# Optimization experiments

Hardware: AMD Instinct MI355X
Metric: run time of the kernel (lower is better)

The kernel has to match this reference:

```python
import jax, jax.numpy as jnp
import numpy as np

B, D, O, I = 64, 128, 512, 512


def setup_inputs() -> dict:
    key = jax.random.key(0)
    k1, k2, k3 = jax.random.split(key, 3)
    inp = jax.random.bernoulli(k1, 0.5, (B, D, I))            # binary activations
    weight_noise = jax.random.bernoulli(k2, 0.5, (D, O, I))   # sigmoid(W) > rand, binary
    # popcount of I fair coins has mean I/2, std sqrt(I)/2; center threshold there
    bias_noise = (I / 2.0 + (jnp.sqrt(I) / 2.0)
                  * jax.random.normal(k3, (D, O), dtype=jnp.float32))
    return {"input": inp, "weight_noise": weight_noise, "bias_noise": bias_noise}


def reference(input, weight_noise, bias_noise):
    # (weight_noise == input).sum(-1) over binary {0,1} tensors equals
    #   dot(w, x) + dot(1-w, 1-x) = I - sum(w) - sum(x) + 2 * dot(w, x)
    # which avoids materializing the (B, D, O, I) comparison tensor.
    x = input.astype(jnp.float32)          # (B, D, I)
    w = weight_noise.astype(jnp.float32)   # (D, O, I)
    dot = jnp.einsum('bdi,doi->bdo', x, w)               # per-direction binary GEMM
    act = (jnp.float32(I) - w.sum(-1)[None, :, :]        # (1, D, O)
           - x.sum(-1)[:, :, None]                        # (B, D, 1)
           + 2.0 * dot)                                   # match counts, (B, D, O)
    return act > bias_noise[None, :, :]                   # bool (B, D, O)
```

## Files before the change

### kernel.cpp

```cpp
#include <hip/hip_runtime.h>
#include <cstdint>

typedef unsigned long long u64;
typedef unsigned int u32;

#define BB 64
#define DD 128
#define OO 512
#define II 512
#define OT 64
#define XROWS (BB * DD)

__device__ __forceinline__ int detect_mode(const u32* __restrict__ w) {
    bool all01 = true, allf = true;
#pragma unroll
    for (int i = 0; i < 32; ++i) {
        u32 v = w[i];
        all01 = all01 && (v <= 1u);
        allf  = allf  && (v == 0u || v == 0x3F800000u);
    }
    return all01 ? 1 : (allf ? 2 : 0);
}

__device__ __forceinline__ u64 pack_row(const void* __restrict__ src,
                                        size_t elem0, int mode, int lane) {
    u64 my = 0;
    if (mode == 0) {
        u64 v = *(const u64*)((const uint8_t*)src + elem0 + (size_t)lane * 8);
#pragma unroll
        for (int j = 0; j < 8; ++j) {
            u64 bj = __ballot(((u32)(v >> (8 * j))) & 1u);
            if (lane == j) my = bj;
        }
    } else {
        const u32 sh = (mode == 1) ? 0u : 23u;
        const uint4* p = (const uint4*)((const u32*)src + elem0);
        uint4 v0 = p[lane];
        uint4 v1 = p[64 + lane];
        u32 b0 = (v0.x >> sh) & 1u, b1 = (v0.y >> sh) & 1u;
        u32 b2 = (v0.z >> sh) & 1u, b3 = (v0.w >> sh) & 1u;
        u32 b4 = (v1.x >> sh) & 1u, b5 = (v1.y >> sh) & 1u;
        u32 b6 = (v1.z >> sh) & 1u, b7 = (v1.w >> sh) & 1u;
        u64 w0 = __ballot(b0), w1 = __ballot(b1), w2 = __ballot(b2), w3 = __ballot(b3);
        u64 w4 = __ballot(b4), w5 = __ballot(b5), w6 = __ballot(b6), w7 = __ballot(b7);
        if (lane == 0) my = w0;  if (lane == 1) my = w1;
        if (lane == 2) my = w2;  if (lane == 3) my = w3;
        if (lane == 4) my = w4;  if (lane == 5) my = w5;
        if (lane == 6) my = w6;  if (lane == 7) my = w7;
    }
    return my;
}

__global__ __launch_bounds__(256)
void pack_x_kernel(const void* __restrict__ x, const void* __restrict__ w,
                   u64* __restrict__ packed) {
    const int gtid = blockIdx.x * 256 + threadIdx.x;
    const int row  = gtid >> 6;
    const int lane = threadIdx.x & 63;
    const int mode = detect_mode((const u32*)w);
    u64 my = pack_row(x, (size_t)row * II, mode, lane);
    if (lane < 8) packed[(size_t)row * 8 + lane] = my;
}

__global__ __launch_bounds__(256)
void fused_kernel(const void* __restrict__ w, const u64* __restrict__ px,
                  const float* __restrict__ bias, int* __restrict__ out) {
    __shared__ u64 wp[OT][9];
    __shared__ u64 xp[BB][8];

    const int tid  = threadIdx.x;
    const int blk  = blockIdx.x;
    const int d    = blk >> 3;
    const int o0   = (blk & 7) * OT;
    const int wv   = tid >> 6;
    const int lane = tid & 63;

    const int mode = detect_mode((const u32*)w);

#pragma unroll
    for (int r = 0; r < 16; ++r) {
        const int o = wv * 16 + r;
        u64 my = pack_row(w, ((size_t)(d * OO + o0 + o)) * II, mode, lane);
        if (lane < 8) wp[o][lane] = my;
    }
#pragma unroll
    for (int t = tid; t < BB * 8; t += 256) {
        int b = t >> 3, k = t & 7;
        xp[b][k] = px[(size_t)(b * DD + d) * 8 + k];
    }
    const float bv = bias[d * OO + o0 + (tid & 63)];
    __syncthreads();

    const int o  = tid & 63;
    const int b0 = (tid >> 6) * 16;

    u64 wr[8];
#pragma unroll
    for (int k = 0; k < 8; ++k) wr[k] = wp[o][k];

    int* outp = out + (size_t)d * OO + o0 + o;
#pragma unroll 4
    for (int bi = 0; bi < 16; ++bi) {
        const int b = b0 + bi;
        int m = 0;
#pragma unroll
        for (int k = 0; k < 8; ++k) m += __popcll(xp[b][k] ^ wr[k]);
        const float act = (float)(512 - m);
        outp[(size_t)b * (DD * OO)] = (act > bv) ? 1 : 0;
    }
}

extern "C" void kernel_launch(void* const* d_in, const int* in_sizes, int n_in,
                              void* d_out, int out_size, void* d_ws, size_t ws_size,
                              hipStream_t stream) {
    const void*  x    = d_in[0];
    const void*  w    = d_in[1];
    const float* bias = (const float*)d_in[2];
    int*         out  = (int*)d_out;
    u64*         px   = (u64*)d_ws;

    pack_x_kernel<<<XROWS / 4, 256, 0, stream>>>(x, w, px);
    fused_kernel<<<DD * (OO / OT), 256, 0, stream>>>(w, px, bias, out);
}
```

Baseline: 39.19 us.

## Fuse input packing into main kernel and remap blocks for XCD locality

Drops the separate pack_x kernel. Each block now packs its own 64 input rows for its direction d straight from global memory, which removes a launch and the round trip through the workspace. Each x row is now packed 8 times, once per o-tile block. To make that redundant read cheaper, block IDs are remapped so the 8 o-tiles of one d land on the same XCD and can share its L2. The added per-block packing work and the extra x reads are the cost.

```diff
diff --git a/kernel.cpp b/kernel.cpp
--- a/kernel.cpp
+++ b/kernel.cpp
@@ -9,7 +9,6 @@
 #define OO 512
 #define II 512
 #define OT 64
-#define XROWS (BB * DD)
 
 __device__ __forceinline__ int detect_mode(const u32* __restrict__ w) {
     bool all01 = true, allf = true;
@@ -52,26 +51,17 @@
 }
 
 __global__ __launch_bounds__(256)
-void pack_x_kernel(const void* __restrict__ x, const void* __restrict__ w,
-                   u64* __restrict__ packed) {
-    const int gtid = blockIdx.x * 256 + threadIdx.x;
-    const int row  = gtid >> 6;
-    const int lane = threadIdx.x & 63;
-    const int mode = detect_mode((const u32*)w);
-    u64 my = pack_row(x, (size_t)row * II, mode, lane);
-    if (lane < 8) packed[(size_t)row * 8 + lane] = my;
-}
-
-__global__ __launch_bounds__(256)
-void fused_kernel(const void* __restrict__ w, const u64* __restrict__ px,
-                  const float* __restrict__ bias, int* __restrict__ out) {
+void binlin_one(const void* __restrict__ x, const void* __restrict__ w,
+                const float* __restrict__ bias, int* __restrict__ out) {
     __shared__ u64 wp[OT][9];
     __shared__ u64 xp[BB][8];
 
     const int tid  = threadIdx.x;
-    const int blk  = blockIdx.x;
-    const int d    = blk >> 3;
-    const int o0   = (blk & 7) * OT;
+    const int bid  = blockIdx.x;
+    const int xcd = bid & 7;
+    const int idx = bid >> 3;
+    const int d   = xcd * 16 + (idx >> 3);
+    const int o0  = (idx & 7) * OT;
     const int wv   = tid >> 6;
     const int lane = tid & 63;
 
@@ -84,9 +74,10 @@
         if (lane < 8) wp[o][lane] = my;
     }
 #pragma unroll
-    for (int t = tid; t < BB * 8; t += 256) {
-        int b = t >> 3, k = t & 7;
-        xp[b][k] = px[(size_t)(b * DD + d) * 8 + k];
+    for (int r = 0; r < 16; ++r) {
+        const int b = wv * 16 + r;
+        u64 my = pack_row(x, ((size_t)(b * DD + d)) * II, mode, lane);
+        if (lane < 8) xp[b][lane] = my;
     }
     const float bv = bias[d * OO + o0 + (tid & 63)];
     __syncthreads();
@@ -117,8 +108,6 @@
     const void*  w    = d_in[1];
     const float* bias = (const float*)d_in[2];
     int*         out  = (int*)d_out;
-    u64*         px   = (u64*)d_ws;
 
-    pack_x_kernel<<<XROWS / 4, 256, 0, stream>>>(x, w, px);
-    fused_kernel<<<DD * (OO / OT), 256, 0, stream>>>(w, px, bias, out);
+    binlin_one<<<DD * (OO / OT), 256, 0, stream>>>(x, w, bias, out);
 }
```

Result: no change. 38.55 us (-1.6%).

## Stage weight tiles into LDS via direct global-to-LDS loads and remap blocks per XCD

Applied to the files above, without the earlier changes.

For byte-encoded inputs, the fused kernel now copies weight rows and packed activations straight into shared memory with global_load_lds in two 16KB halves, then packs bits from LDS using ballots. It also remaps block IDs so consecutive d values stay on the same XCD for L2 locality, and sets an occupancy hint on launch bounds. The goal is fewer per-lane global loads with better coalescing and cache reuse, at the cost of 16KB extra LDS per block, extra barriers, and serialized load/pack phases.

```diff
diff --git a/kernel.cpp b/kernel.cpp
--- a/kernel.cpp
+++ b/kernel.cpp
@@ -22,27 +22,31 @@
     return all01 ? 1 : (allf ? 2 : 0);
 }
 
+__device__ __forceinline__ u64 ballots8_bytes(u64 v, int lane) {
+    u64 keep = 0;
+#pragma unroll
+    for (int j = 0; j < 8; ++j) {
+        u64 bj = __ballot((u32)(v >> (8 * j)) & 1u);
+        if (lane == j) keep = bj;
+    }
+    return keep;
+}
+
 __device__ __forceinline__ u64 pack_row(const void* __restrict__ src,
                                         size_t elem0, int mode, int lane) {
     u64 my = 0;
     if (mode == 0) {
         u64 v = *(const u64*)((const uint8_t*)src + elem0 + (size_t)lane * 8);
-#pragma unroll
-        for (int j = 0; j < 8; ++j) {
-            u64 bj = __ballot(((u32)(v >> (8 * j))) & 1u);
-            if (lane == j) my = bj;
-        }
+        my = ballots8_bytes(v, lane);
     } else {
         const u32 sh = (mode == 1) ? 0u : 23u;
         const uint4* p = (const uint4*)((const u32*)src + elem0);
-        uint4 v0 = p[lane];
-        uint4 v1 = p[64 + lane];
-        u32 b0 = (v0.x >> sh) & 1u, b1 = (v0.y >> sh) & 1u;
-        u32 b2 = (v0.z >> sh) & 1u, b3 = (v0.w >> sh) & 1u;
-        u32 b4 = (v1.x >> sh) & 1u, b5 = (v1.y >> sh) & 1u;
-        u32 b6 = (v1.z >> sh) & 1u, b7 = (v1.w >> sh) & 1u;
-        u64 w0 = __ballot(b0), w1 = __ballot(b1), w2 = __ballot(b2), w3 = __ballot(b3);
-        u64 w4 = __ballot(b4), w5 = __ballot(b5), w6 = __ballot(b6), w7 = __ballot(b7);
+        uint4 a = p[lane];
+        uint4 b = p[64 + lane];
+        u64 w0 = __ballot((a.x >> sh) & 1u), w1 = __ballot((a.y >> sh) & 1u);
+        u64 w2 = __ballot((a.z >> sh) & 1u), w3 = __ballot((a.w >> sh) & 1u);
+        u64 w4 = __ballot((b.x >> sh) & 1u), w5 = __ballot((b.y >> sh) & 1u);
+        u64 w6 = __ballot((b.z >> sh) & 1u), w7 = __ballot((b.w >> sh) & 1u);
         if (lane == 0) my = w0;  if (lane == 1) my = w1;
         if (lane == 2) my = w2;  if (lane == 3) my = w3;
         if (lane == 4) my = w4;  if (lane == 5) my = w5;
@@ -51,45 +55,100 @@
     return my;
 }
 
+__device__ __forceinline__ void gload_lds16(const void* g, void* lds) {
+    __builtin_amdgcn_global_load_lds(
+        (const __attribute__((address_space(1))) void*)g,
+        (__attribute__((address_space(3))) void*)lds, 16, 0, 0);
+}
+
 __global__ __launch_bounds__(256)
 void pack_x_kernel(const void* __restrict__ x, const void* __restrict__ w,
-                   u64* __restrict__ packed) {
+                   u64* __restrict__ px) {
     const int gtid = blockIdx.x * 256 + threadIdx.x;
     const int row  = gtid >> 6;
     const int lane = threadIdx.x & 63;
     const int mode = detect_mode((const u32*)w);
     u64 my = pack_row(x, (size_t)row * II, mode, lane);
-    if (lane < 8) packed[(size_t)row * 8 + lane] = my;
+    if (lane < 8) px[(size_t)row * 8 + lane] = my;
 }
 
-__global__ __launch_bounds__(256)
-void fused_kernel(const void* __restrict__ w, const u64* __restrict__ px,
+__global__ __launch_bounds__(256, 4)
+void fused_kernel(const void* __restrict__ x, const void* __restrict__ w,
+                  const u64* __restrict__ px,
                   const float* __restrict__ bias, int* __restrict__ out) {
+    __shared__ u64 stage64[2048];
     __shared__ u64 wp[OT][9];
     __shared__ u64 xp[BB][8];
 
     const int tid  = threadIdx.x;
-    const int blk  = blockIdx.x;
-    const int d    = blk >> 3;
-    const int o0   = (blk & 7) * OT;
+    const int bid  = blockIdx.x;
+    const int xcd  = bid & 7;
+    const int idx  = bid >> 3;
+    const int d    = xcd * 16 + (idx >> 3);
+    const int o0   = (idx & 7) * OT;
     const int wv   = tid >> 6;
     const int lane = tid & 63;
 
     const int mode = detect_mode((const u32*)w);
+    const float bv = bias[d * OO + o0 + (tid & 63)];
+
+    uint8_t* stage = (uint8_t*)stage64;
+
+    if (mode == 0) {
+        const uint8_t* wtile = (const uint8_t*)w + (size_t)(d * OO + o0) * II;
 
 #pragma unroll
-    for (int r = 0; r < 16; ++r) {
-        const int o = wv * 16 + r;
-        u64 my = pack_row(w, ((size_t)(d * OO + o0 + o)) * II, mode, lane);
-        if (lane < 8) wp[o][lane] = my;
+        for (int i = 0; i < 4; ++i) {
+            const int inst = wv * 4 + i;
+            gload_lds16(wtile + inst * 1024 + lane * 16, stage + inst * 1024);
+        }
+        {
+            const int b = wv * 16 + (lane >> 2);
+            gload_lds16((const uint8_t*)px + ((size_t)(b * DD + d)) * 64
+                                           + (size_t)(lane & 3) * 16,
+                        (uint8_t*)xp + wv * 1024);
+        }
+        asm volatile("s_waitcnt vmcnt(0)" ::: "memory");
+        __syncthreads();
+
+#pragma unroll
+        for (int r = 0; r < 8; ++r) {
+            const int row = wv * 8 + r;
+            u64 v = *(const u64*)(stage + row * 512 + lane * 8);
+            u64 k = ballots8_bytes(v, lane);
+            if (lane < 8) wp[row][lane] = k;
+        }
+        __syncthreads();
+
+#pragma unroll
+        for (int i = 0; i < 4; ++i) {
+            const int inst = wv * 4 + i;
+            gload_lds16(wtile + 16384 + inst * 1024 + lane * 16,
+                        stage + inst * 1024);
+        }
+        asm volatile("s_waitcnt vmcnt(0)" ::: "memory");
+        __syncthreads();
+#pragma unroll
+        for (int r = 0; r < 8; ++r) {
+            const int row = wv * 8 + r;
+            u64 v = *(const u64*)(stage + row * 512 + lane * 8);
+            u64 k = ballots8_bytes(v, lane);
+            if (lane < 8) wp[32 + row][lane] = k;
+        }
+        __syncthreads();
+    } else {
+#pragma unroll
+        for (int r = 0; r < 16; ++r) {
+            const int o = wv * 16 + r;
+            u64 my = pack_row(w, ((size_t)(d * OO + o0 + o)) * II, mode, lane);
+            if (lane < 8) wp[o][lane] = my;
+        }
+        for (int t = tid; t < BB * 8; t += 256) {
+            const int b = t >> 3, k = t & 7;
+            xp[b][k] = px[((size_t)(b * DD + d)) * 8 + k];
+        }
+        __syncthreads();
     }
-#pragma unroll
-    for (int t = tid; t < BB * 8; t += 256) {
-        int b = t >> 3, k = t & 7;
-        xp[b][k] = px[(size_t)(b * DD + d) * 8 + k];
-    }
-    const float bv = bias[d * OO + o0 + (tid & 63)];
-    __syncthreads();
 
     const int o  = tid & 63;
     const int b0 = (tid >> 6) * 16;
@@ -120,5 +179,5 @@
     u64*         px   = (u64*)d_ws;
 
     pack_x_kernel<<<XROWS / 4, 256, 0, stream>>>(x, w, px);
-    fused_kernel<<<DD * (OO / OT), 256, 0, stream>>>(w, px, bias, out);
+    fused_kernel<<<DD * (OO / OT), 256, 0, stream>>>(x, w, px, bias, out);
 }
```

Measured after the change: 38.62 us. Within noise of the previous version (-1.5%).
